# Kernel optimization log

Measured on AMD Instinct MI355X. Metric: run time of the kernel, lower is better.

The kernel has to match this reference:

```python
import jax, jax.numpy as jnp
import numpy as np

EPS = 1e-5  # BatchNorm2d default eps

def setup_inputs() -> dict:
    key = jax.random.key(0)
    k1, k2, k3, k4 = jax.random.split(key, 4)
    B, Cin, Cout, T, V = 64, 64, 128, 300, 25
    x = jax.random.normal(k1, (B, Cin, T, V), dtype=jnp.float32)
    adj = jax.random.uniform(k2, (V, V), dtype=jnp.float32)
    # Conv2d(kernel_size=1) weight (Cout, Cin), kaiming-ish scale
    W = jax.random.normal(k3, (Cout, Cin), dtype=jnp.float32) * (1.0 / np.sqrt(Cin))
    b = jnp.zeros((Cout,), dtype=jnp.float32)
    gamma = jnp.ones((Cout,), dtype=jnp.float32)
    beta = jnp.zeros((Cout,), dtype=jnp.float32)
    return {"x": x, "adj": adj, "W": W, "b": b, "gamma": gamma, "beta": beta}

def reference(x, adj, W, b, gamma, beta):
    # x: (B, C, T, V); graph aggregation over joints: matmul with adj on last dim
    xg = jnp.einsum('bctv,vw->bctw', x, adj)
    # 1x1 conv == per-(t,v) channel projection
    y = jnp.einsum('bctv,oc->botv', xg, W) + b[None, :, None, None]
    # BatchNorm2d (training mode): per-channel stats over (B, T, V), biased var
    mean = jnp.mean(y, axis=(0, 2, 3), keepdims=True)
    var = jnp.mean((y - mean) ** 2, axis=(0, 2, 3), keepdims=True)
    yn = (y - mean) * jax.lax.rsqrt(var + EPS)
    out = jax.nn.relu(gamma[None, :, None, None] * yn + beta[None, :, None, None])
    return out
```

## Files before the change

kernel.cpp:

```cpp
#include <hip/hip_runtime.h>
#include <hip/hip_bf16.h>
#include <stdint.h>

typedef __attribute__((ext_vector_type(8)))  short    short8;
typedef __attribute__((ext_vector_type(16))) float    floatx16;
typedef __attribute__((ext_vector_type(4)))  float    floatx4;
typedef __attribute__((ext_vector_type(4)))  uint32_t uint4v;

#define B_    64
#define CIN   64
#define COUT  128
#define T_    300
#define V_    25
#define NRED  (B_ * T_ * V_)
#define NSLOTS 32
#define NT    12
#define EPS   1e-5f

__device__ __forceinline__ uint32_t pk2(float a, float b) {
    union { __hip_bfloat162 h; uint32_t u; } c;
    c.h = __float22bfloat162_rn(make_float2(a, b));
    return c.u;
}

__device__ __forceinline__ floatx16 fzero16() {
    floatx16 z;
#pragma unroll
    for (int i = 0; i < 16; ++i) z[i] = 0.f;
    return z;
}

__device__ __forceinline__ int div25(int n) { return (n * 5243) >> 17; }

__device__ __forceinline__ void cvt_hb(const floatx16 h, int q, short8 hb[2]) {
    uint32_t pk[8], pp[8];
#pragma unroll
    for (int i = 0; i < 8; ++i) pk[i] = pk2(h[2 * i], h[2 * i + 1]);
#pragma unroll
    for (int i = 0; i < 8; ++i) pp[i] = (uint32_t)__shfl_xor((int)pk[i], 32, 64);
#pragma unroll
    for (int s = 0; s < 2; ++s) {
        union { short8 sv; uint32_t u[4]; } F;
        F.u[0] = q ? pp[4 * s + 2] : pk[4 * s];
        F.u[1] = q ? pp[4 * s + 3] : pk[4 * s + 1];
        F.u[2] = q ? pk[4 * s + 2] : pp[4 * s];
        F.u[3] = q ? pk[4 * s + 3] : pp[4 * s + 1];
        hb[s] = F.sv;
    }
}

__device__ __forceinline__ void build_const_frags(const float* __restrict__ W,
                                                  const float* __restrict__ adj,
                                                  int wave, int ln, int q,
                                                  short8 wf[4], short8 af[2]) {
    const float* wr = W + (32 * wave + ln) * CIN;
#pragma unroll
    for (int kk = 0; kk < 4; ++kk) {
        int c0 = 16 * kk + 8 * q;
        floatx4 a = *(const floatx4*)(wr + c0);
        floatx4 b = *(const floatx4*)(wr + c0 + 4);
        union { short8 sv; uint32_t u[4]; } F;
        F.u[0] = pk2(a[0], a[1]); F.u[1] = pk2(a[2], a[3]);
        F.u[2] = pk2(b[0], b[1]); F.u[3] = pk2(b[2], b[3]);
        wf[kk] = F.sv;
    }
#pragma unroll
    for (int s = 0; s < 2; ++s) {
        union { short8 sv; uint32_t u[4]; } F;
#pragma unroll
        for (int p = 0; p < 4; ++p) {
            int v0 = 16 * s + 8 * q + 2 * p;
            float e0 = (v0     < V_ && ln < V_) ? adj[v0 * V_ + ln]       : 0.f;
            float e1 = (v0 + 1 < V_ && ln < V_) ? adj[(v0 + 1) * V_ + ln] : 0.f;
            F.u[p] = pk2(e0, e1);
        }
        af[s] = F.sv;
    }
}

__device__ __forceinline__ void stage_xT(const float* __restrict__ xb, int t4,
                                         uint32_t* __restrict__ lds, int tid) {
#pragma unroll
    for (int i = 0; i < 4; ++i) {
        int cid = i * 256 + tid;
        if (i < 3 || tid < 32) {
            int ch = cid >> 5;
            int cp = cid & 31;
            const float* p0 = xb + (2 * cp) * 7500 + t4 * 25 + 4 * ch;
            floatx4 a = *(const floatx4*)p0;
            floatx4 b = *(const floatx4*)(p0 + 7500);
            const int g  = cp >> 2;
            const int c2 = cp & 3;
#pragma unroll
            for (int k = 0; k < 4; ++k) {
                int tv = 4 * ch + k;
                lds[tv * 32 + (((g ^ (tv & 7)) << 2) | c2)] = pk2(a[k], b[k]);
            }
        }
    }
}

__device__ __forceinline__ void build_xa_ldsT(const uint32_t* __restrict__ lds,
                                              int tloc, int vcl, int q, short8 xa[4]) {
    const int tv = tloc * 25 + vcl;
    const uint32_t* row = lds + tv * 32;
    const int x7 = tv & 7;
#pragma unroll
    for (int kk = 0; kk < 4; ++kk) {
        union { short8 sv; uint4v u4; } F;
        F.u4 = *(const uint4v*)(row + (((q + 2 * kk) ^ x7) << 2));
        xa[kk] = F.sv;
    }
}

__device__ __forceinline__ floatx16 compute_yt(const short8 xa[4], const short8 wf[4],
                                               const short8 af[2], int q) {
    floatx16 h = fzero16();
#pragma unroll
    for (int kk = 0; kk < 4; ++kk)
        h = __builtin_amdgcn_mfma_f32_32x32x16_bf16(xa[kk], wf[kk], h, 0, 0, 0);
    short8 hb[2];
    cvt_hb(h, q, hb);
    floatx16 y = fzero16();
#pragma unroll
    for (int s = 0; s < 2; ++s)
        y = __builtin_amdgcn_mfma_f32_32x32x16_bf16(af[s], hb[s], y, 0, 0, 0);
    return y;
}

__global__ __launch_bounds__(256, 3) void pass1_kernel(
    const float* __restrict__ x, const float* __restrict__ adj,
    const float* __restrict__ W,
    float* __restrict__ psum, float* __restrict__ psq)
{
    __shared__ __attribute__((aligned(16))) uint32_t ldsx2[3200];

    const int tid  = threadIdx.x;
    const int wave = tid >> 6;
    const int lane = tid & 63;
    const int q    = lane >> 5;
    const int ln   = lane & 31;
    const int b    = blockIdx.y;
    const int tbase = blockIdx.x * NT;

    short8 wf[4], af[2];
    build_const_frags(W, adj, wave, ln, q, wf, af);
    const int vcl = ln < V_ ? ln : V_ - 1;
    const float* xb = x + (size_t)b * (CIN * T_ * V_);

    float sum = 0.f, sq = 0.f;
    for (int g = 0; g < NT / 4; ++g) {
        const int t4 = tbase + 4 * g;
        stage_xT(xb, t4, ldsx2, tid);
        __syncthreads();
#pragma unroll
        for (int tloc = 0; tloc < 4; ++tloc) {
            short8 xa[4];
            build_xa_ldsT(ldsx2, tloc, vcl, q, xa);
            floatx16 y = compute_yt(xa, wf, af, q);
#pragma unroll
            for (int r = 0; r < 16; ++r) { sum += y[r]; sq += y[r] * y[r]; }
        }
        __syncthreads();
    }

    sum += __shfl_xor(sum, 32, 64);
    sq  += __shfl_xor(sq,  32, 64);
    if (q == 0) {
        int slot = (blockIdx.y * 25 + blockIdx.x) & (NSLOTS - 1);
        atomicAdd(&psum[slot * COUT + 32 * wave + ln], sum);
        atomicAdd(&psq [slot * COUT + 32 * wave + ln], sq);
    }
}

__global__ __launch_bounds__(256, 2) void pass2_kernel(
    const float* __restrict__ x, const float* __restrict__ adj,
    const float* __restrict__ W,
    const float* __restrict__ gamma, const float* __restrict__ beta,
    const float* __restrict__ psum, const float* __restrict__ psq,
    float* __restrict__ out)
{
    __shared__ __attribute__((aligned(16))) uint32_t ldsx2[3200];
    __shared__ __attribute__((aligned(16))) float ldso[4][3200];

    const int tid  = threadIdx.x;
    const int wave = tid >> 6;
    const int lane = tid & 63;
    const int q    = lane >> 5;
    const int ln   = lane & 31;
    const int b    = blockIdx.y;
    const int tbase = blockIdx.x * NT;
    const int o_l  = 32 * wave + ln;

    short8 wf[4], af[2];
    build_const_frags(W, adj, wave, ln, q, wf, af);

    float s = 0.f, ss = 0.f;
#pragma unroll 4
    for (int k = 0; k < NSLOTS; ++k) {
        s  += psum[k * COUT + o_l];
        ss += psq [k * COUT + o_l];
    }
    const float mean = s / (float)NRED;
    const float var  = ss / (float)NRED - mean * mean;
    const float inv  = rsqrtf(var + EPS);
    const float sc   = gamma[o_l] * inv;
    const float sh   = beta[o_l] - mean * sc;

    const int vcl = ln < V_ ? ln : V_ - 1;
    const float* xb = x + (size_t)b * (CIN * T_ * V_);
    float* const ob = out + (size_t)(b * COUT + 32 * wave) * (T_ * V_);

    for (int g = 0; g < NT / 4; ++g) {
        const int t4 = tbase + 4 * g;
        stage_xT(xb, t4, ldsx2, tid);
        __syncthreads();

        float* const ow0 = &ldso[wave][ln * 100];
#pragma unroll
        for (int tloc = 0; tloc < 4; ++tloc) {
            short8 xa[4];
            build_xa_ldsT(ldsx2, tloc, vcl, q, xa);
            floatx16 y = compute_yt(xa, wf, af, q);
            float* ow = ow0 + tloc * 25 + 4 * q;
#pragma unroll
            for (int g2 = 0; g2 < 3; ++g2) {
#pragma unroll
                for (int j = 0; j < 4; ++j) {
                    float v = sc * y[4 * g2 + j] + sh;
                    ow[8 * g2 + j] = v > 0.f ? v : 0.f;
                }
            }
            if (q == 0) {
                float v = sc * y[12] + sh;
                ow0[tloc * 25 + 24] = v > 0.f ? v : 0.f;
            }
        }

#pragma unroll
        for (int f = 0; f < 13; ++f) {
            int cid = f * 64 + lane;
            if (f < 12 || lane < 32) {
                int o = div25(cid);
                int c = cid - 25 * o;
                floatx4 v = *(const floatx4*)&ldso[wave][o * 100 + 4 * c];
                *(floatx4*)(ob + (size_t)o * (T_ * V_) + t4 * 25 + 4 * c) = v;
            }
        }
        __syncthreads();
    }
}


extern "C" void kernel_launch(void* const* d_in, const int* in_sizes, int n_in,
                              void* d_out, int out_size, void* d_ws, size_t ws_size,
                              hipStream_t stream) {
    const float* x     = (const float*)d_in[0];
    const float* adj   = (const float*)d_in[1];
    const float* W     = (const float*)d_in[2];
    const float* gamma = (const float*)d_in[4];
    const float* beta  = (const float*)d_in[5];
    float* out = (float*)d_out;

    float* psum = (float*)d_ws;
    float* psq  = (float*)((char*)d_ws + NSLOTS * COUT * sizeof(float));

    hipMemsetAsync(psum, 0, 2 * NSLOTS * COUT * sizeof(float), stream);

    dim3 grid(T_ / NT, B_);
    pass1_kernel<<<grid, 256, 0, stream>>>(x, adj, W, psum, psq);
    pass2_kernel<<<grid, 256, 0, stream>>>(x, adj, W, gamma, beta, psum, psq, out);
}
```

Measured before the change: 454.8 us.

## Double-buffer staged x tiles in LDS with register prefetch in both passes

Splits x staging into a global-load phase into registers and an LDS-commit phase, and double-buffers the LDS tile. The next tile's loads are issued before the MFMA work on the current tile, and one barrier per iteration replaces two. The goal is to hide global load latency behind compute and the output-store loop. The cost is more LDS per block and extra live vector registers for the prefetched data, which could lower occupancy, especially in pass2.

After: 446.4 us. Within noise of the previous version (-1.9%).

```diff
diff --git a/kernel.cpp b/kernel.cpp
--- a/kernel.cpp
+++ b/kernel.cpp
@@ -78,8 +78,8 @@
     }
 }
 
-__device__ __forceinline__ void stage_xT(const float* __restrict__ xb, int t4,
-                                         uint32_t* __restrict__ lds, int tid) {
+__device__ __forceinline__ void stage_issue(const float* __restrict__ xb, int t4,
+                                            int tid, floatx4 a[4], floatx4 b[4]) {
 #pragma unroll
     for (int i = 0; i < 4; ++i) {
         int cid = i * 256 + tid;
@@ -87,14 +87,26 @@
             int ch = cid >> 5;
             int cp = cid & 31;
             const float* p0 = xb + (2 * cp) * 7500 + t4 * 25 + 4 * ch;
-            floatx4 a = *(const floatx4*)p0;
-            floatx4 b = *(const floatx4*)(p0 + 7500);
+            a[i] = *(const floatx4*)p0;
+            b[i] = *(const floatx4*)(p0 + 7500);
+        }
+    }
+}
+
+__device__ __forceinline__ void stage_commit(uint32_t* __restrict__ lds, int tid,
+                                             const floatx4 a[4], const floatx4 b[4]) {
+#pragma unroll
+    for (int i = 0; i < 4; ++i) {
+        int cid = i * 256 + tid;
+        if (i < 3 || tid < 32) {
+            int ch = cid >> 5;
+            int cp = cid & 31;
             const int g  = cp >> 2;
             const int c2 = cp & 3;
 #pragma unroll
             for (int k = 0; k < 4; ++k) {
                 int tv = 4 * ch + k;
-                lds[tv * 32 + (((g ^ (tv & 7)) << 2) | c2)] = pk2(a[k], b[k]);
+                lds[tv * 32 + (((g ^ (tv & 7)) << 2) | c2)] = pk2(a[i][k], b[i][k]);
             }
         }
     }
@@ -133,7 +145,8 @@
     const float* __restrict__ W,
     float* __restrict__ psum, float* __restrict__ psq)
 {
-    __shared__ __attribute__((aligned(16))) uint32_t ldsx2[3200];
+    __shared__ __attribute__((aligned(16))) uint32_t bufA[3200];
+    __shared__ __attribute__((aligned(16))) uint32_t bufB[3200];
 
     const int tid  = threadIdx.x;
     const int wave = tid >> 6;
@@ -148,20 +161,30 @@
     const int vcl = ln < V_ ? ln : V_ - 1;
     const float* xb = x + (size_t)b * (CIN * T_ * V_);
 
+    floatx4 sa[4], sb[4];
+    stage_issue(xb, tbase, tid, sa, sb);
+    stage_commit(bufA, tid, sa, sb);
+    __syncthreads();
+    uint32_t* cur = bufA;
+    uint32_t* nxt = bufB;
+
     float sum = 0.f, sq = 0.f;
     for (int g = 0; g < NT / 4; ++g) {
-        const int t4 = tbase + 4 * g;
-        stage_xT(xb, t4, ldsx2, tid);
-        __syncthreads();
+        if (g < NT / 4 - 1) stage_issue(xb, tbase + 4 * (g + 1), tid, sa, sb);
+        __builtin_amdgcn_sched_barrier(0);
 #pragma unroll
         for (int tloc = 0; tloc < 4; ++tloc) {
             short8 xa[4];
-            build_xa_ldsT(ldsx2, tloc, vcl, q, xa);
+            build_xa_ldsT(cur, tloc, vcl, q, xa);
             floatx16 y = compute_yt(xa, wf, af, q);
 #pragma unroll
             for (int r = 0; r < 16; ++r) { sum += y[r]; sq += y[r] * y[r]; }
         }
-        __syncthreads();
+        if (g < NT / 4 - 1) {
+            stage_commit(nxt, tid, sa, sb);
+            __syncthreads();
+            uint32_t* t = cur; cur = nxt; nxt = t;
+        }
     }
 
     sum += __shfl_xor(sum, 32, 64);
@@ -180,7 +203,8 @@
     const float* __restrict__ psum, const float* __restrict__ psq,
     float* __restrict__ out)
 {
-    __shared__ __attribute__((aligned(16))) uint32_t ldsx2[3200];
+    __shared__ __attribute__((aligned(16))) uint32_t bufA[3200];
+    __shared__ __attribute__((aligned(16))) uint32_t bufB[3200];
     __shared__ __attribute__((aligned(16))) float ldso[4][3200];
 
     const int tid  = threadIdx.x;
@@ -211,16 +235,23 @@
     const float* xb = x + (size_t)b * (CIN * T_ * V_);
     float* const ob = out + (size_t)(b * COUT + 32 * wave) * (T_ * V_);
 
+    floatx4 sa[4], sb[4];
+    stage_issue(xb, tbase, tid, sa, sb);
+    stage_commit(bufA, tid, sa, sb);
+    __syncthreads();
+    uint32_t* cur = bufA;
+    uint32_t* nxt = bufB;
+
     for (int g = 0; g < NT / 4; ++g) {
         const int t4 = tbase + 4 * g;
-        stage_xT(xb, t4, ldsx2, tid);
-        __syncthreads();
+        if (g < NT / 4 - 1) stage_issue(xb, tbase + 4 * (g + 1), tid, sa, sb);
+        __builtin_amdgcn_sched_barrier(0);
 
         float* const ow0 = &ldso[wave][ln * 100];
 #pragma unroll
         for (int tloc = 0; tloc < 4; ++tloc) {
             short8 xa[4];
-            build_xa_ldsT(ldsx2, tloc, vcl, q, xa);
+            build_xa_ldsT(cur, tloc, vcl, q, xa);
             floatx16 y = compute_yt(xa, wf, af, q);
             float* ow = ow0 + tloc * 25 + 4 * q;
 #pragma unroll
@@ -237,6 +268,11 @@
             }
         }
 
+        if (g < NT / 4 - 1) {
+            stage_commit(nxt, tid, sa, sb);
+            __syncthreads();
+        }
+
 #pragma unroll
         for (int f = 0; f < 13; ++f) {
             int cid = f * 64 + lane;
@@ -247,7 +283,8 @@
                 *(floatx4*)(ob + (size_t)o * (T_ * V_) + t4 * 25 + 4 * c) = v;
             }
         }
-        __syncthreads();
+
+        uint32_t* t = cur; cur = nxt; nxt = t;
     }
 }
 
```
